# Kernel tuning notes

Measured on AMD Instinct MI355X. Metric: run time of the kernel, lower is better.

## Reference

```python
import jax, jax.numpy as jnp
import numpy as np

N = 100000       # nodes
E = 1600000      # edges (avg degree 16)
F_IN = 128       # num_features
H = 128          # hidden
C = 10           # num_classes
L = 3            # num_layers
G = 128          # number of graphs in the batch


def setup_inputs() -> dict:
    key = jax.random.key(0)
    ks = jax.random.split(key, 12)
    x = jax.random.normal(ks[0], (N, F_IN), dtype=jnp.float32)
    edge_index = jax.random.randint(ks[1], (2, E), 0, N, dtype=jnp.int64)
    batch = jnp.sort(jax.random.randint(ks[2], (N,), 0, G, dtype=jnp.int64))
    def lin(k, fan_in, fan_out):
        s = 1.0 / np.sqrt(fan_in)
        return jax.random.uniform(k, (fan_in, fan_out), jnp.float32, -s, s)
    w_init = lin(ks[3], F_IN, H)
    b_init = jnp.zeros((H,), jnp.float32)
    w_conv = jnp.stack([lin(ks[4 + i], H, H) for i in range(L - 1)])  # [L-1,H,H]
    b_conv = jnp.zeros((L - 1, H), jnp.float32)
    w_h1 = lin(ks[8], H, H)
    b_h1 = jnp.zeros((H,), jnp.float32)
    w_h2 = lin(ks[9], H, C)
    b_h2 = jnp.zeros((C,), jnp.float32)
    return {"x": x, "edge_index": edge_index, "batch": batch,
            "w_init": w_init, "b_init": b_init,
            "w_conv": w_conv, "b_conv": b_conv,
            "w_h1": w_h1, "b_h1": b_h1, "w_h2": w_h2, "b_h2": b_h2}


def reference(x, edge_index, batch, w_init, b_init, w_conv, b_conv,
              w_h1, b_h1, w_h2, b_h2):
    n = x.shape[0]
    # GCNConv normalization: add self-loops, symmetric deg^-1/2 norm.
    loop = jnp.arange(n, dtype=edge_index.dtype)
    src = jnp.concatenate([edge_index[0], loop])
    dst = jnp.concatenate([edge_index[1], loop])
    deg = jax.ops.segment_sum(jnp.ones_like(dst, x.dtype), dst, num_segments=n)
    dinv = jnp.where(deg > 0, jax.lax.rsqrt(deg), 0.0)
    norm = dinv[src] * dinv[dst]  # [E+N]

    def gcn_conv(h, w, b):
        h = h @ w                                   # [N,H]
        msg = norm[:, None] * h[src]                # gather + scale
        return jax.ops.segment_sum(msg, dst, num_segments=n) + b

    h = jax.nn.relu(gcn_conv(x, w_init, b_init))
    for i in range(w_conv.shape[0]):
        h = jax.nn.relu(gcn_conv(h, w_conv[i], b_conv[i]))

    # global_mean_pool over graph ids
    sums = jax.ops.segment_sum(h, batch, num_segments=G)           # [G,H]
    cnt = jax.ops.segment_sum(jnp.ones((n,), h.dtype), batch, num_segments=G)
    pooled = sums / jnp.maximum(cnt, 1.0)[:, None]

    # classification head (dropout = identity at inference)
    h = jax.nn.relu(pooled @ w_h1 + b_h1)
    logits = h @ w_h2 + b_h2
    return jax.nn.log_softmax(logits, axis=-1)
```

## Files before the change

kernel.cpp:

```cpp
#include <hip/hip_runtime.h>
#include <hip/hip_bf16.h>
#include <math.h>

#define NN 100000
#define EE 1600000
#define HD 128
#define GG 128
#define CC 10

#define BKSH 9
#define NBK  196
#define CH   4096
#define MAXB 12288

typedef __attribute__((ext_vector_type(8))) short short8;
typedef __attribute__((ext_vector_type(4))) float f32x4;
typedef __attribute__((ext_vector_type(2))) float f32x2;

__device__ __forceinline__ unsigned short f2bf(float f) {
    union { float f; unsigned u; } a; a.f = f;
    unsigned r = a.u + 0x7fff + ((a.u >> 16) & 1);
    return (unsigned short)(r >> 16);
}
__device__ __forceinline__ float bfu(unsigned short u) {
    union { unsigned u; float f; } a; a.u = ((unsigned)u) << 16; return a.f;
}

__device__ __forceinline__ unsigned pk4fp8(float f0, float f1, float f2, float f3) {
    unsigned u = 0;
    u = __builtin_amdgcn_cvt_pk_fp8_f32(f0, f1, u, false);
    u = __builtin_amdgcn_cvt_pk_fp8_f32(f2, f3, u, true);
    return u;
}


__global__ __launch_bounds__(256) void k_bhist(const int* __restrict__ dst,
                                               unsigned* __restrict__ bucket_cnt) {
    __shared__ unsigned cnt[256];
    int t = threadIdx.x;
    cnt[t] = 0;
    __syncthreads();
    int base = blockIdx.x * CH;
#pragma unroll
    for (int k = 0; k < 16; ++k) {
        int e = base + k * 256 + t;
        if (e < EE) atomicAdd(&cnt[((unsigned)dst[e]) >> BKSH], 1u);
    }
    __syncthreads();
    if (cnt[t]) atomicAdd(&bucket_cnt[t], cnt[t]);
}

__global__ void k_bscan(const unsigned* __restrict__ bucket_cnt,
                        unsigned* __restrict__ bucket_start,
                        unsigned* __restrict__ cursor, int* __restrict__ row_start) {
    __shared__ unsigned s[256];
    int t = threadIdx.x;
    unsigned v = bucket_cnt[t];
    s[t] = v;
    __syncthreads();
    for (int off = 1; off < 256; off <<= 1) {
        unsigned a = (t >= off) ? s[t - off] : 0;
        __syncthreads();
        s[t] += a;
        __syncthreads();
    }
    unsigned excl = s[t] - v;
    bucket_start[t] = excl;
    cursor[t] = excl;
    if (t == 255) bucket_start[256] = excl + v;
    if (t == 0) row_start[NN] = EE;
}

__global__ __launch_bounds__(256) void k_bscatter(const int* __restrict__ src,
                                                  const int* __restrict__ dst,
                                                  unsigned* __restrict__ cursor,
                                                  unsigned* __restrict__ ebuf) {
    __shared__ unsigned cnt[256], lst[256], gbase[256], ss[256];
    __shared__ unsigned stage[CH];
    __shared__ unsigned char binid[CH];
    int t = threadIdx.x;
    cnt[t] = 0;
    __syncthreads();
    int base = blockIdx.x * CH;
    int nvalid = EE - base; if (nvalid > CH) nvalid = CH;

    unsigned bk[16], rk[16], pv[16];
#pragma unroll
    for (int k = 0; k < 16; ++k) {
        int e = base + k * 256 + t;
        bk[k] = 0xffffffffu;
        if (e < EE) {
            unsigned d = (unsigned)dst[e];
            unsigned b = d >> BKSH;
            pv[k] = (((unsigned)src[e]) << BKSH) | (d & ((1u << BKSH) - 1));
            bk[k] = b;
            rk[k] = atomicAdd(&cnt[b], 1u);
        }
    }
    __syncthreads();
    unsigned v = cnt[t];
    ss[t] = v;
    __syncthreads();
    for (int off = 1; off < 256; off <<= 1) {
        unsigned a = (t >= off) ? ss[t - off] : 0;
        __syncthreads();
        ss[t] += a;
        __syncthreads();
    }
    lst[t] = ss[t] - v;
    if (v) gbase[t] = atomicAdd(&cursor[t], v);
    __syncthreads();
#pragma unroll
    for (int k = 0; k < 16; ++k) {
        if (bk[k] != 0xffffffffu) {
            unsigned slot = lst[bk[k]] + rk[k];
            stage[slot] = pv[k];
            binid[slot] = (unsigned char)bk[k];
        }
    }
    __syncthreads();
    for (int j = t; j < nvalid; j += 256) {
        unsigned b = binid[j];
        ebuf[gbase[b] + (j - lst[b])] = stage[j];
    }
}

__global__ __launch_bounds__(512) void k_bucket_csr(const unsigned* __restrict__ ebuf,
                                                    const unsigned* __restrict__ bucket_start,
                                                    int* __restrict__ row_start,
                                                    float* __restrict__ dinv,
                                                    int* __restrict__ col) {
    __shared__ unsigned degl[512], lst[512], lfill[512], ss[512];
    __shared__ int colstage[MAXB];
    int t = threadIdx.x, b = blockIdx.x;
    unsigned ebase = bucket_start[b];
    int size = (int)(bucket_start[b + 1] - ebase);
    int nbase = b << BKSH;
    degl[t] = 0;
    lfill[t] = 0;
    __syncthreads();
    for (int j = t; j < size; j += 512)
        atomicAdd(&degl[ebuf[ebase + j] & 511u], 1u);
    __syncthreads();
    unsigned v = degl[t];
    ss[t] = v;
    __syncthreads();
    for (int off = 1; off < 512; off <<= 1) {
        unsigned a = (t >= off) ? ss[t - off] : 0;
        __syncthreads();
        ss[t] += a;
        __syncthreads();
    }
    lst[t] = ss[t] - v;
    int node = nbase + t;
    if (node < NN) {
        row_start[node] = (int)(ebase + lst[t]);
        dinv[node] = rsqrtf((float)(v + 1));
    }
    __syncthreads();
    if (size <= MAXB) {
        for (int j = t; j < size; j += 512) {
            unsigned u = ebuf[ebase + j];
            unsigned l = u & 511u;
            unsigned pos = lst[l] + atomicAdd(&lfill[l], 1u);
            colstage[pos] = (int)(u >> BKSH);
        }
        __syncthreads();
        for (int j = t; j < size; j += 512) col[ebase + j] = colstage[j];
    } else {
        for (int j = t; j < size; j += 512) {
            unsigned u = ebuf[ebase + j];
            unsigned l = u & 511u;
            unsigned pos = lst[l] + atomicAdd(&lfill[l], 1u);
            col[ebase + pos] = (int)(u >> BKSH);
        }
    }
}


__global__ void k_prep_w(const float* __restrict__ w0, const float* __restrict__ w1,
                         const float* __restrict__ w2, unsigned short* __restrict__ Wt) {
    int b = blockIdx.x;
    int mat = b >> 6;
    int idx = (b & 63) * 256 + threadIdx.x;
    int k = idx >> 7, n = idx & 127;
    const float* Wm = (mat == 0) ? w0 : ((mat == 1) ? w1 : w2);
    Wt[mat * 16384 + n * 128 + k] = f2bf(Wm[k * 128 + n]);
}


#define LDK 136

template <bool F32IN>
__global__ __launch_bounds__(256) void k_gemm_mfma(
    const void* __restrict__ Ap, const unsigned short* __restrict__ Wt,
    const float* __restrict__ dinv, unsigned* __restrict__ g8) {
    __shared__ unsigned short As[128 * LDK];
    __shared__ unsigned short Ws[128 * LDK];
    __shared__ float dv[128];
    int t = threadIdx.x;
    int r0 = blockIdx.x * 128;

#pragma unroll
    for (int p = 0; p < 8; ++p) {
        int chunk = p * 256 + t;
        int row = chunk >> 4, kc = chunk & 15;
        uint4 sv = make_uint4(0u, 0u, 0u, 0u);
        if (F32IN) {
            const float* A = (const float*)Ap;
            if (r0 + row < NN) {
                const float* ap = A + (size_t)(r0 + row) * HD + kc * 8;
                float4 va = *(const float4*)ap;
                float4 vb = *(const float4*)(ap + 4);
                sv.x = (unsigned)f2bf(va.x) | ((unsigned)f2bf(va.y) << 16);
                sv.y = (unsigned)f2bf(va.z) | ((unsigned)f2bf(va.w) << 16);
                sv.z = (unsigned)f2bf(vb.x) | ((unsigned)f2bf(vb.y) << 16);
                sv.w = (unsigned)f2bf(vb.z) | ((unsigned)f2bf(vb.w) << 16);
            }
        } else {
            const unsigned short* A = (const unsigned short*)Ap;
            if (r0 + row < NN) sv = *(const uint4*)(A + (size_t)(r0 + row) * HD + kc * 8);
        }
        *(uint4*)(As + row * LDK + kc * 8) = sv;
        uint4 w = *(const uint4*)(Wt + (size_t)row * HD + kc * 8);
        *(uint4*)(Ws + row * LDK + kc * 8) = w;
    }
    if (t < 128) dv[t] = (r0 + t < NN) ? dinv[r0 + t] : 0.f;
    __syncthreads();

    int wave = t >> 6, lane = t & 63, quad = lane >> 4, l16 = lane & 15;
    int wr = (wave >> 1) * 64, wc = (wave & 1) * 64;

    f32x4 acc[4][4];
#pragma unroll
    for (int i = 0; i < 4; ++i)
#pragma unroll
        for (int j = 0; j < 4; ++j) acc[i][j] = (f32x4){0.f, 0.f, 0.f, 0.f};

#pragma unroll
    for (int kk = 0; kk < 4; ++kk) {
        int k0 = kk * 32 + quad * 8;
        short8 af[4], bfr[4];
#pragma unroll
        for (int i = 0; i < 4; ++i)
            af[i] = *(const short8*)(As + (wr + i * 16 + l16) * LDK + k0);
#pragma unroll
        for (int j = 0; j < 4; ++j)
            bfr[j] = *(const short8*)(Ws + (wc + j * 16 + l16) * LDK + k0);
#pragma unroll
        for (int i = 0; i < 4; ++i)
#pragma unroll
            for (int j = 0; j < 4; ++j)
                acc[i][j] = __builtin_amdgcn_mfma_f32_16x16x32_bf16(af[i], bfr[j], acc[i][j], 0, 0, 0);
    }
    __syncthreads();

#pragma unroll
    for (int i = 0; i < 4; ++i) {
        int lr = wr + i * 16 + quad * 4;
#pragma unroll
        for (int reg = 0; reg < 4; ++reg) {
            float sc = dv[lr + reg];
#pragma unroll
            for (int j = 0; j < 4; ++j)
                As[(lr + reg) * LDK + wc + j * 16 + l16] = f2bf(acc[i][j][reg] * sc);
        }
    }
    __syncthreads();

    int row = t >> 1, half = t & 1;
    if (r0 + row < NN) {
        const unsigned short* sp = As + row * LDK + half * 64;
        unsigned og[16];
#pragma unroll
        for (int q = 0; q < 16; ++q)
            og[q] = pk4fp8(bfu(sp[4 * q]), bfu(sp[4 * q + 1]),
                           bfu(sp[4 * q + 2]), bfu(sp[4 * q + 3]));
        uint4* dp = (uint4*)(g8 + (size_t)(r0 + row) * 32 + half * 16);
#pragma unroll
        for (int q = 0; q < 4; ++q)
            dp[q] = make_uint4(og[4 * q], og[4 * q + 1], og[4 * q + 2], og[4 * q + 3]);
    }
}


__global__ __launch_bounds__(256) void k_aggregate(
    const unsigned* __restrict__ g8, const int* __restrict__ row_start,
    const int* __restrict__ col, const float* __restrict__ dinv,
    const float* __restrict__ bias, uint2* __restrict__ out) {
    int node = blockIdx.x * 8 + (threadIdx.x >> 5);
    int l = threadIdx.x & 31;
    unsigned su = g8[node * 32 + l];
    f32x2 slo = __builtin_amdgcn_cvt_pk_f32_fp8(su, false);
    f32x2 shi = __builtin_amdgcn_cvt_pk_f32_fp8(su, true);
    float a0 = slo.x, a1 = slo.y, a2 = shi.x, a3 = shi.y;
    int e = row_start[node], end = row_start[node + 1];
    for (; e + 8 <= end; e += 8) {
        int s0 = col[e], s1 = col[e + 1], s2 = col[e + 2], s3 = col[e + 3];
        int s4 = col[e + 4], s5 = col[e + 5], s6 = col[e + 6], s7 = col[e + 7];
        unsigned u0 = g8[s0 * 32 + l];
        unsigned u1 = g8[s1 * 32 + l];
        unsigned u2 = g8[s2 * 32 + l];
        unsigned u3 = g8[s3 * 32 + l];
        unsigned u4 = g8[s4 * 32 + l];
        unsigned u5 = g8[s5 * 32 + l];
        unsigned u6 = g8[s6 * 32 + l];
        unsigned u7 = g8[s7 * 32 + l];
#pragma unroll
        for (int k = 0; k < 8; ++k) {
            unsigned u = (k == 0) ? u0 : (k == 1) ? u1 : (k == 2) ? u2 : (k == 3) ? u3
                       : (k == 4) ? u4 : (k == 5) ? u5 : (k == 6) ? u6 : u7;
            f32x2 lo = __builtin_amdgcn_cvt_pk_f32_fp8(u, false);
            f32x2 hi = __builtin_amdgcn_cvt_pk_f32_fp8(u, true);
            a0 += lo.x; a1 += lo.y; a2 += hi.x; a3 += hi.y;
        }
    }
    for (; e < end; ++e) {
        unsigned u = g8[col[e] * 32 + l];
        f32x2 lo = __builtin_amdgcn_cvt_pk_f32_fp8(u, false);
        f32x2 hi = __builtin_amdgcn_cvt_pk_f32_fp8(u, true);
        a0 += lo.x; a1 += lo.y; a2 += hi.x; a3 += hi.y;
    }
    float sc = dinv[node];
    float4 bb = ((const float4*)bias)[l];
    float r0 = fmaxf(fmaf(a0, sc, bb.x), 0.f);
    float r1 = fmaxf(fmaf(a1, sc, bb.y), 0.f);
    float r2 = fmaxf(fmaf(a2, sc, bb.z), 0.f);
    float r3 = fmaxf(fmaf(a3, sc, bb.w), 0.f);
    uint2 o;
    o.x = (unsigned)f2bf(r0) | ((unsigned)f2bf(r1) << 16);
    o.y = (unsigned)f2bf(r2) | ((unsigned)f2bf(r3) << 16);
    out[node * 32 + l] = o;
}


__device__ __forceinline__ int lower_bound_i(const int* a, int n, int key) {
    int lo = 0, hi = n;
    while (lo < hi) {
        int mid = (lo + hi) >> 1;
        if (a[mid] < key) lo = mid + 1;
        else hi = mid;
    }
    return lo;
}

__global__ __launch_bounds__(512) void k_poolhead(
    const unsigned short* __restrict__ h, const int* __restrict__ batch,
    const float* __restrict__ w1, const float* __restrict__ b1,
    const float* __restrict__ w2, const float* __restrict__ b2,
    float* __restrict__ out) {
    __shared__ float partial[4][HD];
    __shared__ float pooled[HD], hrow[HD], logits[CC];
    __shared__ int range[2];
    int t = threadIdx.x, g = blockIdx.x;
    if (t == 0) {
        range[0] = lower_bound_i(batch, NN, g);
        range[1] = lower_bound_i(batch, NN, g + 1);
    }
    __syncthreads();
    int lo = range[0], hi = range[1];
    int feat = t & 127, sl = t >> 7;
    float acc = 0.f;
    for (int r = lo + sl; r < hi; r += 4) acc += bfu(h[(size_t)r * HD + feat]);
    partial[sl][feat] = acc;
    __syncthreads();
    if (t < HD) {
        float s = partial[0][t] + partial[1][t] + partial[2][t] + partial[3][t];
        pooled[t] = s / fmaxf((float)(hi - lo), 1.f);
    }
    __syncthreads();
    if (t < HD) {
        float a = b1[t];
        for (int k = 0; k < HD; ++k) a = fmaf(pooled[k], w1[k * HD + t], a);
        hrow[t] = fmaxf(a, 0.f);
    }
    __syncthreads();
    if (t < CC) {
        float a = b2[t];
        for (int k = 0; k < HD; ++k) a = fmaf(hrow[k], w2[k * CC + t], a);
        logits[t] = a;
    }
    __syncthreads();
    if (t < CC) {
        float m = logits[0];
        for (int i = 1; i < CC; ++i) m = fmaxf(m, logits[i]);
        float s = 0.f;
        for (int i = 0; i < CC; ++i) s += expf(logits[i] - m);
        out[g * CC + t] = logits[t] - m - logf(s);
    }
}


extern "C" void kernel_launch(void* const* d_in, const int* in_sizes, int n_in,
                              void* d_out, int out_size, void* d_ws, size_t ws_size,
                              hipStream_t stream) {
    const float* x      = (const float*)d_in[0];
    const int*   ei     = (const int*)d_in[1];
    const int*   batch  = (const int*)d_in[2];
    const float* w_init = (const float*)d_in[3];
    const float* b_init = (const float*)d_in[4];
    const float* w_conv = (const float*)d_in[5];
    const float* b_conv = (const float*)d_in[6];
    const float* w_h1   = (const float*)d_in[7];
    const float* b_h1   = (const float*)d_in[8];
    const float* w_h2   = (const float*)d_in[9];
    const float* b_h2   = (const float*)d_in[10];
    float* out = (float*)d_out;
    (void)n_in; (void)in_sizes; (void)out_size; (void)ws_size;

    char* ws = (char*)d_ws;
    size_t off = 0;
    auto alloc = [&](size_t bytes) -> void* {
        void* p = ws + off;
        off += (bytes + 255) & ~(size_t)255;
        return p;
    };
    unsigned short* hAbf         = (unsigned short*)alloc((size_t)NN * HD * 2);
    unsigned*       g8           = (unsigned*)alloc((size_t)NN * 32 * 4);
    unsigned short* Wt           = (unsigned short*)alloc(3 * 16384 * 2);
    float*          dinv         = (float*)alloc((size_t)NN * 4);
    int*            row_start    = (int*)alloc((size_t)(NN + 1) * 4);
    int*            col          = (int*)alloc((size_t)EE * 4);
    unsigned*       ebuf         = (unsigned*)alloc((size_t)EE * 4);
    unsigned*       bucket_cnt   = (unsigned*)alloc(256 * 4);
    unsigned*       bucket_start = (unsigned*)alloc(257 * 4);
    unsigned*       cursor       = (unsigned*)alloc(256 * 4);

    const int* srcp = ei;
    const int* dstp = ei + EE;

    hipMemsetAsync(bucket_cnt, 0, 256 * 4, stream);

    int nchunks = (EE + CH - 1) / CH;
    k_bhist<<<nchunks, 256, 0, stream>>>(dstp, bucket_cnt);
    k_bscan<<<1, 256, 0, stream>>>(bucket_cnt, bucket_start, cursor, row_start);
    k_bscatter<<<nchunks, 256, 0, stream>>>(srcp, dstp, cursor, ebuf);
    k_bucket_csr<<<NBK, 512, 0, stream>>>(ebuf, bucket_start, row_start, dinv, col);

    k_prep_w<<<192, 256, 0, stream>>>(w_init, w_conv, w_conv + HD * HD, Wt);

    int gemm_grid = (NN + 127) / 128;
    int agg_grid = NN / 8;

    k_gemm_mfma<true><<<gemm_grid, 256, 0, stream>>>(x, Wt, dinv, g8);
    k_aggregate<<<agg_grid, 256, 0, stream>>>(g8, row_start, col, dinv, b_init, (uint2*)hAbf);
    k_gemm_mfma<false><<<gemm_grid, 256, 0, stream>>>(hAbf, Wt + 16384, dinv, g8);
    k_aggregate<<<agg_grid, 256, 0, stream>>>(g8, row_start, col, dinv, b_conv, (uint2*)hAbf);
    k_gemm_mfma<false><<<gemm_grid, 256, 0, stream>>>(hAbf, Wt + 2 * 16384, dinv, g8);
    k_aggregate<<<agg_grid, 256, 0, stream>>>(g8, row_start, col, dinv, b_conv + HD, (uint2*)hAbf);

    k_poolhead<<<GG, 512, 0, stream>>>(hAbf, batch, w_h1, b_h1, w_h2, b_h2, out);
}
```

Measured before the change: 405.6 us.

## Split mean-pool into row-chunk partial sums with atomics plus separate head kernel

Replaces the one-block-per-graph pooling kernel, which did serial binary searches and scanned about 780 rows per block using only 128 blocks, with a pool kernel launched over 782 row chunks. Each chunk accumulates runs of identical graph ids and flushes them into global sums and counts with atomics. A second small kernel then normalises the pooled rows and runs the MLP head and log-softmax. This is meant to spread the pooling read over many more blocks, at the cost of two memsets, an extra launch, and atomic float adds whose ordering makes results nondeterministic.

Result: faster. 379.5 us (-6.4%).

```diff
diff --git a/kernel.cpp b/kernel.cpp
--- a/kernel.cpp
+++ b/kernel.cpp
@@ -334,46 +334,48 @@
 }
 
 
-__device__ __forceinline__ int lower_bound_i(const int* a, int n, int key) {
-    int lo = 0, hi = n;
-    while (lo < hi) {
-        int mid = (lo + hi) >> 1;
-        if (a[mid] < key) lo = mid + 1;
-        else hi = mid;
-    }
-    return lo;
-}
-
-__global__ __launch_bounds__(512) void k_poolhead(
+__global__ __launch_bounds__(256) void k_pool_partial(
     const unsigned short* __restrict__ h, const int* __restrict__ batch,
-    const float* __restrict__ w1, const float* __restrict__ b1,
-    const float* __restrict__ w2, const float* __restrict__ b2,
-    float* __restrict__ out) {
-    __shared__ float partial[4][HD];
-    __shared__ float pooled[HD], hrow[HD], logits[CC];
-    __shared__ int range[2];
-    int t = threadIdx.x, g = blockIdx.x;
-    if (t == 0) {
-        range[0] = lower_bound_i(batch, NN, g);
-        range[1] = lower_bound_i(batch, NN, g + 1);
-    }
-    __syncthreads();
-    int lo = range[0], hi = range[1];
-    int feat = t & 127, sl = t >> 7;
+    float* __restrict__ pooled, float* __restrict__ cntg) {
+    int t = threadIdx.x;
+    int slot = t >> 7, feat = t & 127;
+    int base = blockIdx.x * 128;
+    int endr = base + 128; if (endr > NN) endr = NN;
     float acc = 0.f;
-    for (int r = lo + sl; r < hi; r += 4) acc += bfu(h[(size_t)r * HD + feat]);
-    partial[sl][feat] = acc;
-    __syncthreads();
-    if (t < HD) {
-        float s = partial[0][t] + partial[1][t] + partial[2][t] + partial[3][t];
-        pooled[t] = s / fmaxf((float)(hi - lo), 1.f);
-    }
-    __syncthreads();
-    if (t < HD) {
-        float a = b1[t];
-        for (int k = 0; k < HD; ++k) a = fmaf(pooled[k], w1[k * HD + t], a);
-        hrow[t] = fmaxf(a, 0.f);
-    }
+    int cur = -1, run = 0;
+    for (int r = base + slot; r < endr; r += 2) {
+        int g = batch[r];
+        float v = bfu(h[(size_t)r * HD + feat]);
+        if (g != cur) {
+            if (cur >= 0) {
+                atomicAdd(&pooled[cur * HD + feat], acc);
+                if (feat == 0) atomicAdd(&cntg[cur], (float)run);
+            }
+            cur = g; acc = 0.f; run = 0;
+        }
+        acc += v; ++run;
+    }
+    if (cur >= 0) {
+        atomicAdd(&pooled[cur * HD + feat], acc);
+        if (feat == 0) atomicAdd(&cntg[cur], (float)run);
+    }
+}
+
+
+__global__ __launch_bounds__(128) void k_head(const float* __restrict__ pooled,
+                                              const float* __restrict__ cntg,
+                                              const float* __restrict__ w1,
+                                              const float* __restrict__ b1,
+                                              const float* __restrict__ w2,
+                                              const float* __restrict__ b2,
+                                              float* __restrict__ out) {
+    __shared__ float row[HD], hrow[HD], logits[CC];
+    int g = blockIdx.x, t = threadIdx.x;
+    row[t] = pooled[g * HD + t] / fmaxf(cntg[g], 1.f);
+    __syncthreads();
+    float acc = b1[t];
+    for (int k = 0; k < HD; ++k) acc = fmaf(row[k], w1[k * HD + t], acc);
+    hrow[t] = fmaxf(acc, 0.f);
     __syncthreads();
     if (t < CC) {
         float a = b2[t];
@@ -425,11 +427,15 @@
     unsigned*       bucket_cnt   = (unsigned*)alloc(256 * 4);
     unsigned*       bucket_start = (unsigned*)alloc(257 * 4);
     unsigned*       cursor       = (unsigned*)alloc(256 * 4);
+    float*          pooled       = (float*)alloc((size_t)GG * HD * 4);
+    float*          cntg         = (float*)alloc((size_t)GG * 4);
 
     const int* srcp = ei;
     const int* dstp = ei + EE;
 
     hipMemsetAsync(bucket_cnt, 0, 256 * 4, stream);
+    hipMemsetAsync(pooled, 0, (size_t)GG * HD * 4, stream);
+    hipMemsetAsync(cntg, 0, (size_t)GG * 4, stream);
 
     int nchunks = (EE + CH - 1) / CH;
     k_bhist<<<nchunks, 256, 0, stream>>>(dstp, bucket_cnt);
@@ -449,5 +455,6 @@
     k_gemm_mfma<false><<<gemm_grid, 256, 0, stream>>>(hAbf, Wt + 2 * 16384, dinv, g8);
     k_aggregate<<<agg_grid, 256, 0, stream>>>(g8, row_start, col, dinv, b_conv + HD, (uint2*)hAbf);
 
-    k_poolhead<<<GG, 512, 0, stream>>>(hAbf, batch, w_h1, b_h1, w_h2, b_h2, out);
-}
+    k_pool_partial<<<(NN + 127) / 128, 256, 0, stream>>>(hAbf, batch, pooled, cntg);
+    k_head<<<GG, 128, 0, stream>>>(pooled, cntg, w_h1, b_h1, w_h2, b_h2, out);
+}
```
